# Kernel tuning notes

Hardware: AMD Instinct MI355X
Metric: run time of the kernel (lower is better)

The kernel has to match this reference:

```python
import jax, jax.numpy as jnp
import numpy as np

B, H, W, C = 8, 28, 28, 1024
NH = 16
HD = C // NH          # head dim 64
HID = 4 * C           # mlp hidden 4096
BC = C // 2           # bottleneck channels 512
SCALE = HD ** -0.5


def setup_inputs() -> dict:
    key = jax.random.key(0)
    ks = iter(jax.random.split(key, 32))
    def rn(shape, s=0.02):
        return jax.random.normal(next(ks), shape, jnp.float32) * s
    return dict(
        x=jax.random.normal(next(ks), (B, H, W, C), jnp.float32),
        norm1_w=jnp.ones((C,), jnp.float32), norm1_b=jnp.zeros((C,), jnp.float32),
        qkv_w=rn((C, 3 * C)), qkv_b=jnp.zeros((3 * C,), jnp.float32),
        proj_w=rn((C, C)), proj_b=jnp.zeros((C,), jnp.float32),
        rel_h=rn((2 * H - 1, HD)), rel_w=rn((2 * W - 1, HD)),
        norm2_w=jnp.ones((C,), jnp.float32), norm2_b=jnp.zeros((C,), jnp.float32),
        fc1_w=rn((C, HID)), fc1_b=jnp.zeros((HID,), jnp.float32),
        fc2_w=rn((HID, C)), fc2_b=jnp.zeros((C,), jnp.float32),
        conv1_w=rn((1, 1, C, BC)), ln1_w=jnp.ones((BC,), jnp.float32), ln1_b=jnp.zeros((BC,), jnp.float32),
        conv2_w=rn((3, 3, BC, BC)), ln2_w=jnp.ones((BC,), jnp.float32), ln2_b=jnp.zeros((BC,), jnp.float32),
        conv3_w=rn((1, 1, BC, C)), ln3_w=rn((C,)), ln3_b=rn((C,)),
    )


def _ln(x, w, b, eps):
    # layernorm over last axis (channels in NHWC)
    m = jnp.mean(x, -1, keepdims=True)
    v = jnp.mean((x - m) ** 2, -1, keepdims=True)
    return (x - m) * jax.lax.rsqrt(v + eps) * w + b


def _conv(x, w, pad):
    return jax.lax.conv_general_dilated(
        x, w, (1, 1), pad, dimension_numbers=('NHWC', 'HWIO', 'NHWC'))


def _gelu(x):
    return jax.nn.gelu(x, approximate=False)


def _block_forward(x, norm1_w, norm1_b, qkv_w, qkv_b, proj_w, proj_b,
                   rel_h, rel_w, norm2_w, norm2_b, fc1_w, fc1_b, fc2_w, fc2_b,
                   conv1_w, ln1_w, ln1_b, conv2_w, ln2_w, ln2_b, conv3_w, ln3_w, ln3_b):
    S = H * W
    shortcut = x
    xn = _ln(x, norm1_w, norm1_b, 1e-5)

    # ---- attention with decomposed relative position bias ----
    qkv = xn.reshape(B, S, C) @ qkv_w + qkv_b                 # [B,S,3C]
    qkv = qkv.reshape(B, S, 3, NH, HD).transpose(2, 0, 3, 1, 4)  # [3,B,nh,S,hd]
    q, k, v = qkv[0], qkv[1], qkv[2]
    attn = jnp.einsum('bnsd,bntd->bnst', q * SCALE, k)        # [B,nh,S,S]

    idx_h = jnp.arange(H)[:, None] - jnp.arange(H)[None, :] + (H - 1)
    idx_w = jnp.arange(W)[:, None] - jnp.arange(W)[None, :] + (W - 1)
    Rh = rel_h[idx_h]   # [H,H,hd]
    Rw = rel_w[idx_w]   # [W,W,hd]
    qr = q.reshape(B, NH, H, W, HD)
    bias_h = jnp.einsum('bnhwd,hkd->bnhwk', qr, Rh)           # [B,nh,H,W,H]
    bias_w = jnp.einsum('bnhwd,wkd->bnhwk', qr, Rw)           # [B,nh,H,W,W]
    attn = (attn.reshape(B, NH, H, W, H, W)
            + bias_h[..., :, None] + bias_w[..., None, :]).reshape(B, NH, S, S)

    attn = jax.nn.softmax(attn, axis=-1)
    out = jnp.einsum('bnst,bntd->bnsd', attn, v)              # [B,nh,S,hd]
    out = out.transpose(0, 2, 1, 3).reshape(B, H, W, C)
    out = out @ proj_w + proj_b

    x = shortcut + out

    # ---- MLP ----
    xn = _ln(x, norm2_w, norm2_b, 1e-5)
    x = x + (_gelu(xn.reshape(B, S, C) @ fc1_w + fc1_b) @ fc2_w + fc2_b).reshape(B, H, W, C)

    # ---- residual bottleneck conv (channel LayerNorm, eps=1e-6) ----
    out = _conv(x, conv1_w, 'VALID')
    out = _gelu(_ln(out, ln1_w, ln1_b, 1e-6))
    out = _conv(out, conv2_w, ((1, 1), (1, 1)))
    out = _gelu(_ln(out, ln2_w, ln2_b, 1e-6))
    out = _conv(out, conv3_w, 'VALID')
    out = _ln(out, ln3_w, ln3_b, 1e-6)
    return x + out


def reference(x, norm1_w, norm1_b, qkv_w, qkv_b, proj_w, proj_b,
              rel_h, rel_w, norm2_w, norm2_b, fc1_w, fc1_b, fc2_w, fc2_b,
              conv1_w, ln1_w, ln1_b, conv2_w, ln2_w, ln2_b, conv3_w, ln3_w, ln3_b):
    return _block_forward(x, norm1_w, norm1_b, qkv_w, qkv_b, proj_w, proj_b,
                          rel_h, rel_w, norm2_w, norm2_b, fc1_w, fc1_b, fc2_w, fc2_b,
                          conv1_w, ln1_w, ln1_b, conv2_w, ln2_w, ln2_b, conv3_w, ln3_w, ln3_b)
```

## Files before the change

### kernel.cpp

```cpp
#include <hip/hip_runtime.h>
#include <cstdint>
#include <cstddef>

using u16 = unsigned short;
using u32 = unsigned int;

__device__ __forceinline__ float bf2f(u16 u){
  union { u32 i; float f; } x; x.i = ((u32)u) << 16; return x.f;
}
__device__ __forceinline__ u16 f2bf(float f){
  union { float f; u32 i; } x; x.f = f;
  u32 r = x.i + 0x7fffu + ((x.i >> 16) & 1u);
  return (u16)(r >> 16);
}
__device__ __forceinline__ float gelu_f(float x){
  return 0.5f * x * (1.0f + erff(x * 0.70710678118654752f));
}
__device__ __forceinline__ void gld16(const void* g, void* l){
  __builtin_amdgcn_global_load_lds((__attribute__((address_space(1))) void*)(void*)g,
                                   (__attribute__((address_space(3))) void*)l, 16, 0, 0);
}

typedef __bf16 bf16x8 __attribute__((ext_vector_type(8)));
typedef float  f32x4  __attribute__((ext_vector_type(4)));
typedef u16    u16x4  __attribute__((ext_vector_type(4)));

__global__ __launch_bounds__(256) void k_transpose(const float* __restrict__ src,
                                                   u16* __restrict__ dst, int R, int C){
  __shared__ u16 tile[32][33];
  int bx = blockIdx.x * 32;
  int by = blockIdx.y * 32;
  int tx = threadIdx.x & 31;
  int ty = threadIdx.x >> 5;
  for (int r = ty; r < 32; r += 8)
    tile[r][tx] = f2bf(src[(size_t)(by + r) * C + bx + tx]);
  __syncthreads();
  for (int r = ty; r < 32; r += 8)
    dst[(size_t)(bx + r) * R + by + tx] = tile[tx][r];
}

template<bool IN_F32, bool DO_GELU>
__global__ __launch_bounds__(256) void k_layernorm(const void* __restrict__ inp,
    const float* __restrict__ w, const float* __restrict__ bsh,
    u16* __restrict__ out, int cols, float eps){
  int row = blockIdx.x, t = threadIdx.x;
  size_t base = (size_t)row * cols;
  const float* inf = (const float*)inp;
  const u16*  inb = (const u16*)inp;
  float v[4];
  int ep = cols >> 8;
  float s = 0.f, ss = 0.f;
  for (int e = 0; e < ep; ++e){
    int idx = t + (e << 8);
    float x = IN_F32 ? inf[base + idx] : bf2f(inb[base + idx]);
    v[e] = x; s += x; ss += x * x;
  }
#pragma unroll
  for (int off = 1; off < 64; off <<= 1){
    s  += __shfl_xor(s, off, 64);
    ss += __shfl_xor(ss, off, 64);
  }
  __shared__ float red[8];
  int wv = t >> 6;
  if ((t & 63) == 0){ red[wv] = s; red[4 + wv] = ss; }
  __syncthreads();
  s  = red[0] + red[1] + red[2] + red[3];
  ss = red[4] + red[5] + red[6] + red[7];
  float inv = 1.f / (float)cols;
  float mean = s * inv;
  float var = ss * inv - mean * mean;
  float rs = rsqrtf(var + eps);
  for (int e = 0; e < ep; ++e){
    int idx = t + (e << 8);
    float y = (v[e] - mean) * rs * w[idx] + bsh[idx];
    if (DO_GELU) y = gelu_f(y);
    out[base + idx] = f2bf(y);
  }
}

__global__ __launch_bounds__(256) void k_final(const u16* __restrict__ c3,
    const u16* __restrict__ x2, const float* __restrict__ w,
    const float* __restrict__ bsh, float* __restrict__ out){
  int row = blockIdx.x, t = threadIdx.x;
  size_t base = (size_t)row << 10;
  float v[4];
  float s = 0.f, ss = 0.f;
#pragma unroll
  for (int e = 0; e < 4; ++e){
    int idx = t + (e << 8);
    float x = bf2f(c3[base + idx]);
    v[e] = x; s += x; ss += x * x;
  }
#pragma unroll
  for (int off = 1; off < 64; off <<= 1){
    s  += __shfl_xor(s, off, 64);
    ss += __shfl_xor(ss, off, 64);
  }
  __shared__ float red[8];
  int wv = t >> 6;
  if ((t & 63) == 0){ red[wv] = s; red[4 + wv] = ss; }
  __syncthreads();
  s  = red[0] + red[1] + red[2] + red[3];
  ss = red[4] + red[5] + red[6] + red[7];
  float mean = s * (1.f/1024.f);
  float var = ss * (1.f/1024.f) - mean * mean;
  float rs = rsqrtf(var + 1e-6f);
#pragma unroll
  for (int e = 0; e < 4; ++e){
    int idx = t + (e << 8);
    float y = (v[e] - mean) * rs * w[idx] + bsh[idx];
    out[base + idx] = bf2f(x2[base + idx]) + y;
  }
}

template<bool BIAS, bool GELU, bool RES, bool OUTB, bool OUTF>
__global__ __launch_bounds__(256, 2) void k_gemm(
    const u16* __restrict__ A, const u16* __restrict__ Bt,
    const float* __restrict__ bias, const float* __restrict__ resf,
    u16* __restrict__ outb, float* __restrict__ outf, int N, int K)
{
  __shared__ __align__(16) u16 As[128 * 32];
  __shared__ __align__(16) u16 Bs[128 * 32];
  int t = threadIdx.x, lane = t & 63, wv = t >> 6;

  int nbx = gridDim.x;
  int nwg = nbx * gridDim.y;
  int li  = blockIdx.y * nbx + blockIdx.x;
  int qc = nwg >> 3, rc = nwg & 7;
  int xcd = li & 7, jj = li >> 3;
  int wg = (xcd < rc ? xcd * (qc + 1) : rc * (qc + 1) + (xcd - rc) * qc) + jj;
  int byy = wg / nbx;
  int bxx = wg - byy * nbx;
  int m0 = byy << 7, n0 = bxx << 7;

  int wm = (wv >> 1) << 6, wn = (wv & 1) << 6;

  f32x4 acc[4][4];
  const f32x4 z4 = {0.f, 0.f, 0.f, 0.f};
#pragma unroll
  for (int i = 0; i < 4; ++i)
#pragma unroll
    for (int j = 0; j < 4; ++j) acc[i][j] = z4;

  int srow = (wv << 5) + (lane >> 2);
  int skp  = (lane & 3) << 3;
  const u16* Ag = A  + (size_t)(m0 + srow) * K + skp;
  const u16* Bg = Bt + (size_t)(n0 + srow) * K + skp;
  u16* As0 = &As[(wv << 5) * 32];
  u16* As1 = As0 + 16 * 32;
  u16* Bs0 = &Bs[(wv << 5) * 32];
  u16* Bs1 = Bs0 + 16 * 32;
  const size_t rowskip = (size_t)16 * K;

  int fr = lane & 15, fq = (lane >> 4) << 3;

  for (int k0 = 0; k0 < K; k0 += 32){
    gld16(Ag + k0, As0);
    gld16(Ag + rowskip + k0, As1);
    gld16(Bg + k0, Bs0);
    gld16(Bg + rowskip + k0, Bs1);
    __syncthreads();
    bf16x8 af[4], bfr[4];
#pragma unroll
    for (int i = 0; i < 4; ++i)
      af[i] = *(const bf16x8*)&As[(wm + i * 16 + fr) * 32 + fq];
#pragma unroll
    for (int j = 0; j < 4; ++j)
      bfr[j] = *(const bf16x8*)&Bs[(wn + j * 16 + fr) * 32 + fq];
#pragma unroll
    for (int i = 0; i < 4; ++i)
#pragma unroll
      for (int j = 0; j < 4; ++j)
        acc[i][j] = __builtin_amdgcn_mfma_f32_16x16x32_bf16(af[i], bfr[j], acc[i][j], 0, 0, 0);
    __syncthreads();
  }

  int rr = (lane >> 4) << 2;
  int cc = lane & 15;
#pragma unroll
  for (int i = 0; i < 4; ++i)
#pragma unroll
    for (int j = 0; j < 4; ++j){
      int gc = n0 + wn + j * 16 + cc;
      float bb = BIAS ? bias[gc] : 0.f;
#pragma unroll
      for (int r = 0; r < 4; ++r){
        int gr = m0 + wm + i * 16 + rr + r;
        size_t idx = (size_t)gr * N + gc;
        float vv = acc[i][j][r] + bb;
        if (RES) vv += resf[idx];
        if (GELU) vv = gelu_f(vv);
        if (OUTF) outf[idx] = vv;
        if (OUTB) outb[idx] = f2bf(vv);
      }
    }
}

__global__ __launch_bounds__(256) void k_vtrans(const u16* __restrict__ qkv, u16* __restrict__ vtg){
  __shared__ u32 tile[64][33];
  int bnh = blockIdx.x;
  int st  = blockIdx.y;
  int b = bnh >> 4, nh = bnh & 15;
  int t = threadIdx.x;
  int tx = t & 31;
  int ty = t >> 5;
  const u16* src = qkv + (size_t)b * 784 * 3072 + 2048 + nh * 64;
  int s0 = st << 6;
  for (int r = ty; r < 64; r += 8){
    int s = s0 + r;
    u32 val = 0u;
    if (s < 784) val = *(const u32*)(src + (size_t)s * 3072 + tx * 2);
    tile[r][tx] = val;
  }
  __syncthreads();
  u16* dst = vtg + (size_t)bnh * 64 * 832 + s0;
  for (int d = ty; d < 64; d += 8){
    u32 lo = tile[2 * tx][d >> 1];
    u32 hi = tile[2 * tx + 1][d >> 1];
    u16 a  = (d & 1) ? (u16)(lo >> 16) : (u16)lo;
    u16 bb = (d & 1) ? (u16)(hi >> 16) : (u16)hi;
    u32 pk = (u32)a | ((u32)bb << 16);
    *(u32*)(dst + (size_t)d * 832 + 2 * tx) = pk;
  }
}

#define PST 72
#define GSTR 132
#define LOG2E 1.4426950408889634f
__global__ __launch_bounds__(256, 3) void k_attn7(const u16* __restrict__ qkv,
    const float* __restrict__ relh, const float* __restrict__ relw,
    const u16* __restrict__ vtg, u16* __restrict__ out)
{
  __shared__ __align__(16) u16 k_s[64 * 64];
  __shared__ __align__(16) u16 v_s[64 * 64];
  __shared__ __align__(16) u16 p_s[128 * PST];
  __shared__ __align__(16) u16 gh_t[28 * GSTR];
  __shared__ __align__(16) u16 gw_t[28 * GSTR];

  const int t = threadIdx.x, lane = t & 63, wv = t >> 6;
  int id = blockIdx.x;
  int xr = id & 7, rest = id >> 3;
  int qt = rest % 7, gg = rest / 7;
  int bnh = xr + (gg << 3);
  const int b = bnh >> 4, nh = bnh & 15;
  const int q0 = qt << 7;
  const size_t rowbase = (size_t)b * 784;
  const int wq0 = wv << 5;
  const int fr = lane & 15;
  const int fq = lane >> 4;

  u16* rh_s = p_s;
  u16* rw_s = p_s + 64 * PST;
  {
    int row = t >> 2, c0 = (t & 3) << 4;
    u16 bh_[16], bw_[16];
    if (row < 55){
      const float* ph = relh + row * 64 + c0;
      const float* pw = relw + row * 64 + c0;
#pragma unroll
      for (int e = 0; e < 16; ++e){ bh_[e] = f2bf(ph[e]); bw_[e] = f2bf(pw[e]); }
    } else {
#pragma unroll
      for (int e = 0; e < 16; ++e){ bh_[e] = 0; bw_[e] = 0; }
    }
    *(uint4*)&rh_s[row * PST + c0]     = *(uint4*)bh_;
    *(uint4*)&rh_s[row * PST + c0 + 8] = *(uint4*)(bh_ + 8);
    *(uint4*)&rw_s[row * PST + c0]     = *(uint4*)bw_;
    *(uint4*)&rw_s[row * PST + c0 + 8] = *(uint4*)(bw_ + 8);
  }

  bf16x8 qf[2][2];
#pragma unroll
  for (int mf = 0; mf < 2; ++mf)
#pragma unroll
    for (int ks = 0; ks < 2; ++ks){
      int row = q0 + wq0 + mf * 16 + fr;
      if (row < 784){
        qf[mf][ks] = *(const bf16x8*)(qkv + (rowbase + row) * 3072 + nh * 64 + fq * 8 + ks * 32);
      } else {
        uint4 z = {0u,0u,0u,0u}; qf[mf][ks] = *(bf16x8*)&z;
      }
    }
  __syncthreads();

  const f32x4 z4 = {0.f,0.f,0.f,0.f};
#pragma unroll
  for (int which = 0; which < 2; ++which){
    const u16* rs = which ? rw_s : rh_s;
    f32x4 G[2][4];
#pragma unroll
    for (int mf = 0; mf < 2; ++mf)
#pragma unroll
      for (int nf = 0; nf < 4; ++nf) G[mf][nf] = z4;
#pragma unroll
    for (int nf = 0; nf < 4; ++nf){
      bf16x8 rf0 = *(const bf16x8*)&rs[(nf * 16 + fr) * PST + fq * 8];
      bf16x8 rf1 = *(const bf16x8*)&rs[(nf * 16 + fr) * PST + fq * 8 + 32];
#pragma unroll
      for (int mf = 0; mf < 2; ++mf){
        G[mf][nf] = __builtin_amdgcn_mfma_f32_16x16x32_bf16(qf[mf][0], rf0, G[mf][nf], 0, 0, 0);
        G[mf][nf] = __builtin_amdgcn_mfma_f32_16x16x32_bf16(qf[mf][1], rf1, G[mf][nf], 0, 0, 0);
      }
    }
    u16* gt = which ? gw_t : gh_t;
#pragma unroll
    for (int mf = 0; mf < 2; ++mf)
#pragma unroll
      for (int r = 0; r < 4; ++r){
        int lr = wq0 + mf * 16 + fq * 4 + r;
        int grow = q0 + lr;
        int hq = grow / 28;
        int coord = which ? (grow - hq * 28) : hq;
#pragma unroll
        for (int nf = 0; nf < 4; ++nf){
          int j = nf * 16 + fr;
          int kk = coord + 27 - j;
          if ((unsigned)kk < 28u) gt[kk * GSTR + lr] = f2bf(G[mf][nf][r] * LOG2E);
        }
      }
  }
  __syncthreads();

  f32x4 acc[2][5];
#pragma unroll
  for (int mf = 0; mf < 2; ++mf)
#pragma unroll
    for (int nf = 0; nf < 5; ++nf) acc[mf][nf] = z4;

  u16 onesu[8];
#pragma unroll
  for (int e = 0; e < 8; ++e) onesu[e] = 0x3f80;
  bf16x8 onesf = *(bf16x8*)onesu;

  const int sr = lane >> 3;
  const int sc = (lane & 7) ^ sr;
  const u16* kstage = qkv + rowbase * 3072 + 1024 + nh * 64;
  const u16* vstage = vtg + (size_t)bnh * 64 * 832;
  const int r0 = (wv << 4) + sr;
  u16* kd0 = &k_s[(wv << 4) * 64];
  u16* kd1 = &k_s[((wv << 4) + 8) * 64];
  u16* vd0 = &v_s[(wv << 4) * 64];
  u16* vd1 = &v_s[((wv << 4) + 8) * 64];
  const int swz = (fr & 7);

  const float SSC = 0.125f * LOG2E;

  for (int kt = 0; kt < 13; ++kt){
    const int ktb = kt << 6;
    __syncthreads();
    {
      int jg0 = ktb + r0;       int jc0 = jg0 < 784 ? jg0 : 783;
      int jg1 = jg0 + 8;        int jc1 = jg1 < 784 ? jg1 : 783;
      gld16(kstage + (size_t)jc0 * 3072 + (sc << 3), kd0);
      gld16(kstage + (size_t)jc1 * 3072 + (sc << 3), kd1);
      gld16(vstage + (size_t)r0 * 832 + ktb + (sc << 3), vd0);
      gld16(vstage + (size_t)(r0 + 8) * 832 + ktb + (sc << 3), vd1);
    }
    __syncthreads();

    f32x4 S[2][4];
#pragma unroll
    for (int nf = 0; nf < 4; ++nf){
      int rb = (nf * 16 + fr) << 6;
      bf16x8 kf0 = *(const bf16x8*)&k_s[rb + ((fq ^ swz) << 3)];
      bf16x8 kf1 = *(const bf16x8*)&k_s[rb + (((fq + 4) ^ swz) << 3)];
#pragma unroll
      for (int mf = 0; mf < 2; ++mf){
        f32x4 s = z4;
        s = __builtin_amdgcn_mfma_f32_16x16x32_bf16(qf[mf][0], kf0, s, 0, 0, 0);
        s = __builtin_amdgcn_mfma_f32_16x16x32_bf16(qf[mf][1], kf1, s, 0, 0, 0);
        S[mf][nf] = s;
      }
    }

    int hj[4], wj[4]; bool val[4];
#pragma unroll
    for (int nf = 0; nf < 4; ++nf){
      int jg = ktb + nf * 16 + fr;
      int h = jg / 28;
      hj[nf] = h; wj[nf] = jg - h * 28; val[nf] = (jg < 784);
    }

#pragma unroll
    for (int mf = 0; mf < 2; ++mf){
      int lrb = wq0 + mf * 16 + fq * 4;
#pragma unroll
      for (int nf = 0; nf < 4; ++nf){
        u16x4 h4 = *(const u16x4*)&gh_t[hj[nf] * GSTR + lrb];
        u16x4 w4 = *(const u16x4*)&gw_t[wj[nf] * GSTR + lrb];
#pragma unroll
        for (int r = 0; r < 4; ++r){
          float p = 0.f;
          if (val[nf])
            p = exp2f(fmaf(SSC, S[mf][nf][r], bf2f(h4[r]) + bf2f(w4[r])));
          p_s[(lrb + r) * PST + nf * 16 + fr] = f2bf(p);
        }
      }
    }

#pragma unroll
    for (int ks = 0; ks < 2; ++ks){
      bf16x8 pf0 = *(const bf16x8*)&p_s[(wq0 + fr) * PST + fq * 8 + ks * 32];
      bf16x8 pf1 = *(const bf16x8*)&p_s[(wq0 + 16 + fr) * PST + fq * 8 + ks * 32];
#pragma unroll
      for (int nf = 0; nf < 4; ++nf){
        bf16x8 vf = *(const bf16x8*)&v_s[((nf * 16 + fr) << 6) + (((fq + ks * 4) ^ swz) << 3)];
        acc[0][nf] = __builtin_amdgcn_mfma_f32_16x16x32_bf16(pf0, vf, acc[0][nf], 0, 0, 0);
        acc[1][nf] = __builtin_amdgcn_mfma_f32_16x16x32_bf16(pf1, vf, acc[1][nf], 0, 0, 0);
      }
      acc[0][4] = __builtin_amdgcn_mfma_f32_16x16x32_bf16(pf0, onesf, acc[0][4], 0, 0, 0);
      acc[1][4] = __builtin_amdgcn_mfma_f32_16x16x32_bf16(pf1, onesf, acc[1][4], 0, 0, 0);
    }
  }

#pragma unroll
  for (int mf = 0; mf < 2; ++mf)
#pragma unroll
    for (int r = 0; r < 4; ++r){
      int row = q0 + wq0 + mf * 16 + fq * 4 + r;
      if (row < 784){
        float inv = 1.f / acc[mf][4][r];
        u16* dp = out + (rowbase + row) * 1024 + nh * 64 + fr;
#pragma unroll
        for (int nf = 0; nf < 4; ++nf)
          dp[nf * 16] = f2bf(acc[mf][nf][r] * inv);
      }
    }
}

__global__ __launch_bounds__(256) void k_im2col(const u16* __restrict__ g, u16* __restrict__ im){
  int idx = blockIdx.x * 256 + threadIdx.x;
  int p  = idx / 576;
  int c8 = idx - p * 576;
  int k0 = c8 << 3;
  int t9 = k0 >> 9;
  int ci = k0 & 511;
  int ky = t9 / 3, kx = t9 - ky * 3;
  int bb = p / 784;
  int s = p - bb * 784;
  int h = s / 28, w = s - h * 28;
  int hh = h + ky - 1, ww = w + kx - 1;
  uint4 val = make_uint4(0u, 0u, 0u, 0u);
  if ((unsigned)hh < 28u && (unsigned)ww < 28u)
    val = *(const uint4*)&g[(((size_t)(bb * 28 + hh)) * 28 + ww) * 512 + ci];
  *(uint4*)&im[(size_t)p * 4608 + k0] = val;
}

extern "C" void kernel_launch(void* const* d_in, const int* in_sizes, int n_in,
                              void* d_out, int out_size, void* d_ws, size_t ws_size,
                              hipStream_t stream)
{
  (void)in_sizes; (void)n_in; (void)out_size; (void)ws_size;
  const float* x      = (const float*)d_in[0];
  const float* n1w    = (const float*)d_in[1];
  const float* n1b    = (const float*)d_in[2];
  const float* qkv_w  = (const float*)d_in[3];
  const float* qkv_b  = (const float*)d_in[4];
  const float* proj_w = (const float*)d_in[5];
  const float* proj_b = (const float*)d_in[6];
  const float* rel_h  = (const float*)d_in[7];
  const float* rel_w  = (const float*)d_in[8];
  const float* n2w    = (const float*)d_in[9];
  const float* n2b    = (const float*)d_in[10];
  const float* fc1_w  = (const float*)d_in[11];
  const float* fc1_b  = (const float*)d_in[12];
  const float* fc2_w  = (const float*)d_in[13];
  const float* fc2_b  = (const float*)d_in[14];
  const float* c1w    = (const float*)d_in[15];
  const float* l1w    = (const float*)d_in[16];
  const float* l1b    = (const float*)d_in[17];
  const float* c2w    = (const float*)d_in[18];
  const float* l2w    = (const float*)d_in[19];
  const float* l2b    = (const float*)d_in[20];
  const float* c3w    = (const float*)d_in[21];
  const float* l3w    = (const float*)d_in[22];
  const float* l3b    = (const float*)d_in[23];

  char* ws = (char*)d_ws;
  size_t off = 0;
  auto alloc = [&](size_t bytes) -> void* {
    void* p = ws + off; off += (bytes + 255) & ~(size_t)255; return p;
  };
  const size_t M = 6272;
  u16* qkvT  = (u16*)alloc((size_t)3072 * 1024 * 2);
  u16* projT = (u16*)alloc((size_t)1024 * 1024 * 2);
  u16* fc1T  = (u16*)alloc((size_t)4096 * 1024 * 2);
  u16* fc2T  = (u16*)alloc((size_t)1024 * 4096 * 2);
  u16* c1T   = (u16*)alloc((size_t)512 * 1024 * 2);
  u16* c2T   = (u16*)alloc((size_t)512 * 4608 * 2);
  u16* c3T   = (u16*)alloc((size_t)1024 * 512 * 2);
  u16* qkvbuf = (u16*)alloc(M * 3072 * 2);
  u16* attn   = (u16*)alloc(M * 1024 * 2);
  u16* xn     = (u16*)alloc(M * 1024 * 2);
  float* x1   = (float*)alloc(M * 1024 * 4);
  u16* x2b    = (u16*)alloc(M * 1024 * 2);
  u16* c1buf  = (u16*)alloc(M * 512 * 2);
  u16* g1buf  = (u16*)alloc(M * 512 * 2);
  u16* hmlp   = qkvbuf;
  u16* im     = qkvbuf;
  u16* xn2    = xn;
  u16* c2buf  = c1buf;
  u16* g2buf  = g1buf;
  u16* c3buf  = attn;
  u16* vtg    = (u16*)x1;

  dim3 blk(256);
  k_transpose<<<dim3(3072/32, 1024/32), blk, 0, stream>>>(qkv_w, qkvT, 1024, 3072);
  k_transpose<<<dim3(1024/32, 1024/32), blk, 0, stream>>>(proj_w, projT, 1024, 1024);
  k_transpose<<<dim3(4096/32, 1024/32), blk, 0, stream>>>(fc1_w, fc1T, 1024, 4096);
  k_transpose<<<dim3(1024/32, 4096/32), blk, 0, stream>>>(fc2_w, fc2T, 4096, 1024);
  k_transpose<<<dim3(512/32, 1024/32),  blk, 0, stream>>>(c1w, c1T, 1024, 512);
  k_transpose<<<dim3(512/32, 4608/32),  blk, 0, stream>>>(c2w, c2T, 4608, 512);
  k_transpose<<<dim3(1024/32, 512/32),  blk, 0, stream>>>(c3w, c3T, 512, 1024);

  k_layernorm<true,false><<<6272, blk, 0, stream>>>(x, n1w, n1b, xn, 1024, 1e-5f);
  k_gemm<true,false,false,true,false><<<dim3(24,49), blk, 0, stream>>>(
      xn, qkvT, qkv_b, nullptr, qkvbuf, nullptr, 3072, 1024);
  k_vtrans<<<dim3(128, 13), blk, 0, stream>>>(qkvbuf, vtg);
  k_attn7<<<896, blk, 0, stream>>>(qkvbuf, rel_h, rel_w, vtg, attn);
  k_gemm<true,false,true,false,true><<<dim3(8,49), blk, 0, stream>>>(
      attn, projT, proj_b, x, nullptr, x1, 1024, 1024);
  k_layernorm<true,false><<<6272, blk, 0, stream>>>(x1, n2w, n2b, xn2, 1024, 1e-5f);
  k_gemm<true,true,false,true,false><<<dim3(32,49), blk, 0, stream>>>(
      xn2, fc1T, fc1_b, nullptr, hmlp, nullptr, 4096, 1024);
  k_gemm<true,false,true,true,false><<<dim3(8,49), blk, 0, stream>>>(
      hmlp, fc2T, fc2_b, x1, x2b, nullptr, 1024, 4096);
  k_gemm<false,false,false,true,false><<<dim3(4,49), blk, 0, stream>>>(
      x2b, c1T, nullptr, nullptr, c1buf, nullptr, 512, 1024);
  k_layernorm<false,true><<<6272, blk, 0, stream>>>(c1buf, l1w, l1b, g1buf, 512, 1e-6f);
  k_im2col<<<14112, blk, 0, stream>>>(g1buf, im);
  k_gemm<false,false,false,true,false><<<dim3(4,49), blk, 0, stream>>>(
      im, c2T, nullptr, nullptr, c2buf, nullptr, 512, 4608);
  k_layernorm<false,true><<<6272, blk, 0, stream>>>(c2buf, l2w, l2b, g2buf, 512, 1e-6f);
  k_gemm<false,false,false,true,false><<<dim3(8,49), blk, 0, stream>>>(
      g2buf, c3T, nullptr, nullptr, c3buf, nullptr, 1024, 512);
  k_final<<<6272, blk, 0, stream>>>(c3buf, x2b, l3w, l3b, (float*)d_out);
}
```

Before: 725.6 us.

## Double-buffer GEMM LDS loads, fuse im2col into conv GEMM, stage bf16 epilogue

The GEMM kernel now stages K-tiles into two LDS buffers, so the global-to-LDS loads for the next tile overlap the MFMA work on the current one. Waits use explicit vmcnt waitcnts and raw barriers. The 3x3 conv GEMM now builds its im2col addresses on the fly, reading padded taps from a zeroed scratch buffer, so the separate im2col kernel and its large intermediate buffer go away. Bf16 outputs are written through an LDS tile with 16-byte coalesced stores. The costs are double the LDS use, per-tile address arithmetic in the conv path, and an extra barrier in the epilogue.

```diff
diff --git a/kernel.cpp b/kernel.cpp
--- a/kernel.cpp
+++ b/kernel.cpp
@@ -113,14 +113,16 @@
   }
 }
 
-template<bool BIAS, bool GELU, bool RES, bool OUTB, bool OUTF>
+template<int DEPTH, bool BIAS, bool GELU, bool RES, bool OUTB, bool OUTF, bool CONV>
 __global__ __launch_bounds__(256, 2) void k_gemm(
     const u16* __restrict__ A, const u16* __restrict__ Bt,
     const float* __restrict__ bias, const float* __restrict__ resf,
-    u16* __restrict__ outb, float* __restrict__ outf, int N, int K)
+    u16* __restrict__ outb, float* __restrict__ outf,
+    const u16* __restrict__ zb, int N, int K)
 {
-  __shared__ __align__(16) u16 As[128 * 32];
-  __shared__ __align__(16) u16 Bs[128 * 32];
+  __shared__ __align__(16) u16 smem[DEPTH * 2 * 128 * 32];
+  u16* Asb = smem;
+  u16* Bsb = smem + DEPTH * 4096;
   int t = threadIdx.x, lane = t & 63, wv = t >> 6;
 
   int nbx = gridDim.x;
@@ -146,20 +148,44 @@
   int skp  = (lane & 3) << 3;
   const u16* Ag = A  + (size_t)(m0 + srow) * K + skp;
   const u16* Bg = Bt + (size_t)(n0 + srow) * K + skp;
-  u16* As0 = &As[(wv << 5) * 32];
-  u16* As1 = As0 + 16 * 32;
-  u16* Bs0 = &Bs[(wv << 5) * 32];
-  u16* Bs1 = Bs0 + 16 * 32;
   const size_t rowskip = (size_t)16 * K;
 
+  int bb0 = 0, h0 = 0, w0 = 0, bb1 = 0, h1 = 0, w1 = 0;
+  if (CONV){
+    int p0 = m0 + srow;
+    bb0 = p0 / 784; int s0i = p0 - bb0 * 784; h0 = s0i / 28; w0 = s0i - h0 * 28;
+    int p1 = p0 + 16;
+    bb1 = p1 / 784; int s1i = p1 - bb1 * 784; h1 = s1i / 28; w1 = s1i - h1 * 28;
+  }
+
   int fr = lane & 15, fq = (lane >> 4) << 3;
 
-  for (int k0 = 0; k0 < K; k0 += 32){
-    gld16(Ag + k0, As0);
-    gld16(Ag + rowskip + k0, As1);
-    gld16(Bg + k0, Bs0);
-    gld16(Bg + rowskip + k0, Bs1);
-    __syncthreads();
+  auto stage = [&](int buf, int k0){
+    u16* a0 = Asb + buf * 4096 + (wv << 5) * 32;
+    u16* b0 = Bsb + buf * 4096 + (wv << 5) * 32;
+    if (CONV){
+      int tap = k0 >> 9;
+      int ky = tap / 3, kx = tap - ky * 3;
+      int ci = (k0 & 511) + skp;
+      int hh0 = h0 + ky - 1, ww0 = w0 + kx - 1;
+      int hh1 = h1 + ky - 1, ww1 = w1 + kx - 1;
+      const u16* s0 = ((unsigned)hh0 < 28u && (unsigned)ww0 < 28u)
+          ? A + (((size_t)(bb0 * 28 + hh0)) * 28 + ww0) * 512 + ci : zb;
+      const u16* s1 = ((unsigned)hh1 < 28u && (unsigned)ww1 < 28u)
+          ? A + (((size_t)(bb1 * 28 + hh1)) * 28 + ww1) * 512 + ci : zb;
+      gld16(s0, a0);
+      gld16(s1, a0 + 16 * 32);
+    } else {
+      gld16(Ag + k0, a0);
+      gld16(Ag + rowskip + k0, a0 + 16 * 32);
+    }
+    gld16(Bg + k0, b0);
+    gld16(Bg + rowskip + k0, b0 + 16 * 32);
+  };
+
+  auto compute = [&](int buf){
+    const u16* As = Asb + buf * 4096;
+    const u16* Bs = Bsb + buf * 4096;
     bf16x8 af[4], bfr[4];
 #pragma unroll
     for (int i = 0; i < 4; ++i)
@@ -172,28 +198,70 @@
 #pragma unroll
       for (int j = 0; j < 4; ++j)
         acc[i][j] = __builtin_amdgcn_mfma_f32_16x16x32_bf16(af[i], bfr[j], acc[i][j], 0, 0, 0);
-    __syncthreads();
+  };
+
+  int nk = K >> 5;
+  stage(0, 0);
+
+  for (int kk = 0; kk < nk; ++kk){
+    int nxt = kk + 1;
+    if (nxt < nk){
+      stage(nxt & 1, nxt << 5);
+      asm volatile("s_waitcnt vmcnt(4)" ::: "memory");
+    } else {
+      asm volatile("s_waitcnt vmcnt(0)" ::: "memory");
+    }
+    __builtin_amdgcn_s_barrier();
+    compute(kk & 1);
+    __builtin_amdgcn_s_barrier();
   }
 
   int rr = (lane >> 4) << 2;
   int cc = lane & 15;
-#pragma unroll
-  for (int i = 0; i < 4; ++i)
-#pragma unroll
-    for (int j = 0; j < 4; ++j){
-      int gc = n0 + wn + j * 16 + cc;
-      float bb = BIAS ? bias[gc] : 0.f;
-#pragma unroll
-      for (int r = 0; r < 4; ++r){
-        int gr = m0 + wm + i * 16 + rr + r;
-        size_t idx = (size_t)gr * N + gc;
-        float vv = acc[i][j][r] + bb;
-        if (RES) vv += resf[idx];
-        if (GELU) vv = gelu_f(vv);
-        if (OUTF) outf[idx] = vv;
-        if (OUTB) outb[idx] = f2bf(vv);
-      }
-    }
+  if (OUTB){
+    u16* Cs = smem;
+#pragma unroll
+    for (int i = 0; i < 4; ++i)
+#pragma unroll
+      for (int j = 0; j < 4; ++j){
+        int lc = wn + j * 16 + cc;
+        int gc = n0 + lc;
+        float bb = BIAS ? bias[gc] : 0.f;
+#pragma unroll
+        for (int r = 0; r < 4; ++r){
+          int lr = wm + i * 16 + rr + r;
+          float vv = acc[i][j][r] + bb;
+          if (RES) vv += resf[(size_t)(m0 + lr) * N + gc];
+          if (GELU) vv = gelu_f(vv);
+          Cs[lr * 128 + lc] = f2bf(vv);
+        }
+      }
+    __syncthreads();
+#pragma unroll
+    for (int it = 0; it < 8; ++it){
+      int flat = it * 256 + t;
+      int row = flat >> 4;
+      int col = (flat & 15) << 3;
+      *(uint4*)&outb[(size_t)(m0 + row) * N + n0 + col] = *(const uint4*)&Cs[row * 128 + col];
+    }
+  } else {
+#pragma unroll
+    for (int i = 0; i < 4; ++i)
+#pragma unroll
+      for (int j = 0; j < 4; ++j){
+        int gc = n0 + wn + j * 16 + cc;
+        float bb = BIAS ? bias[gc] : 0.f;
+#pragma unroll
+        for (int r = 0; r < 4; ++r){
+          int gr = m0 + wm + i * 16 + rr + r;
+          size_t idx = (size_t)gr * N + gc;
+          float vv = acc[i][j][r] + bb;
+          if (RES) vv += resf[idx];
+          if (GELU) vv = gelu_f(vv);
+          outf[idx] = vv;
+        }
+      }
+  }
 }
 
 __global__ __launch_bounds__(256) void k_vtrans(const u16* __restrict__ qkv, u16* __restrict__ vtg){
@@ -426,24 +494,6 @@
           dp[nf * 16] = f2bf(acc[mf][nf][r] * inv);
       }
     }
-}
-
-__global__ __launch_bounds__(256) void k_im2col(const u16* __restrict__ g, u16* __restrict__ im){
-  int idx = blockIdx.x * 256 + threadIdx.x;
-  int p  = idx / 576;
-  int c8 = idx - p * 576;
-  int k0 = c8 << 3;
-  int t9 = k0 >> 9;
-  int ci = k0 & 511;
-  int ky = t9 / 3, kx = t9 - ky * 3;
-  int bb = p / 784;
-  int s = p - bb * 784;
-  int h = s / 28, w = s - h * 28;
-  int hh = h + ky - 1, ww = w + kx - 1;
-  uint4 val = make_uint4(0u, 0u, 0u, 0u);
-  if ((unsigned)hh < 28u && (unsigned)ww < 28u)
-    val = *(const uint4*)&g[(((size_t)(bb * 28 + hh)) * 28 + ww) * 512 + ci];
-  *(uint4*)&im[(size_t)p * 4608 + k0] = val;
 }
 
 extern "C" void kernel_launch(void* const* d_in, const int* in_sizes, int n_in,
@@ -496,13 +546,15 @@
   u16* x2b    = (u16*)alloc(M * 1024 * 2);
   u16* c1buf  = (u16*)alloc(M * 512 * 2);
   u16* g1buf  = (u16*)alloc(M * 512 * 2);
+  u16* zbuf   = (u16*)alloc(256);
   u16* hmlp   = qkvbuf;
-  u16* im     = qkvbuf;
   u16* xn2    = xn;
   u16* c2buf  = c1buf;
   u16* g2buf  = g1buf;
   u16* c3buf  = attn;
   u16* vtg    = (u16*)x1;
+
+  hipMemsetAsync(zbuf, 0, 256, stream);
 
   dim3 blk(256);
   k_transpose<<<dim3(3072/32, 1024/32), blk, 0, stream>>>(qkv_w, qkvT, 1024, 3072);
@@ -514,25 +566,24 @@
   k_transpose<<<dim3(1024/32, 512/32),  blk, 0, stream>>>(c3w, c3T, 512, 1024);
 
   k_layernorm<true,false><<<6272, blk, 0, stream>>>(x, n1w, n1b, xn, 1024, 1e-5f);
-  k_gemm<true,false,false,true,false><<<dim3(24,49), blk, 0, stream>>>(
-      xn, qkvT, qkv_b, nullptr, qkvbuf, nullptr, 3072, 1024);
+  k_gemm<2,true,false,false,true,false,false><<<dim3(24,49), blk, 0, stream>>>(
+      xn, qkvT, qkv_b, nullptr, qkvbuf, nullptr, nullptr, 3072, 1024);
   k_vtrans<<<dim3(128, 13), blk, 0, stream>>>(qkvbuf, vtg);
   k_attn7<<<896, blk, 0, stream>>>(qkvbuf, rel_h, rel_w, vtg, attn);
-  k_gemm<true,false,true,false,true><<<dim3(8,49), blk, 0, stream>>>(
-      attn, projT, proj_b, x, nullptr, x1, 1024, 1024);
+  k_gemm<2,true,false,true,false,true,false><<<dim3(8,49), blk, 0, stream>>>(
+      attn, projT, proj_b, x, nullptr, x1, nullptr, 1024, 1024);
   k_layernorm<true,false><<<6272, blk, 0, stream>>>(x1, n2w, n2b, xn2, 1024, 1e-5f);
-  k_gemm<true,true,false,true,false><<<dim3(32,49), blk, 0, stream>>>(
-      xn2, fc1T, fc1_b, nullptr, hmlp, nullptr, 4096, 1024);
-  k_gemm<true,false,true,true,false><<<dim3(8,49), blk, 0, stream>>>(
-      hmlp, fc2T, fc2_b, x1, x2b, nullptr, 1024, 4096);
-  k_gemm<false,false,false,true,false><<<dim3(4,49), blk, 0, stream>>>(
-      x2b, c1T, nullptr, nullptr, c1buf, nullptr, 512, 1024);
+  k_gemm<2,true,true,false,true,false,false><<<dim3(32,49), blk, 0, stream>>>(
+      xn2, fc1T, fc1_b, nullptr, hmlp, nullptr, nullptr, 4096, 1024);
+  k_gemm<2,true,false,true,true,false,false><<<dim3(8,49), blk, 0, stream>>>(
+      hmlp, fc2T, fc2_b, x1, x2b, nullptr, nullptr, 1024, 4096);
+  k_gemm<2,false,false,false,true,false,false><<<dim3(4,49), blk, 0, stream>>>(
+      x2b, c1T, nullptr, nullptr, c1buf, nullptr, nullptr, 512, 1024);
   k_layernorm<false,true><<<6272, blk, 0, stream>>>(c1buf, l1w, l1b, g1buf, 512, 1e-6f);
-  k_im2col<<<14112, blk, 0, stream>>>(g1buf, im);
-  k_gemm<false,false,false,true,false><<<dim3(4,49), blk, 0, stream>>>(
-      im, c2T, nullptr, nullptr, c2buf, nullptr, 512, 4608);
+  k_gemm<2,false,false,false,true,false,true><<<dim3(4,49), blk, 0, stream>>>(
+      g1buf, c2T, nullptr, nullptr, c2buf, nullptr, zbuf, 512, 4608);
   k_layernorm<false,true><<<6272, blk, 0, stream>>>(c2buf, l2w, l2b, g2buf, 512, 1e-6f);
-  k_gemm<false,false,false,true,false><<<dim3(8,49), blk, 0, stream>>>(
-      g2buf, c3T, nullptr, nullptr, c3buf, nullptr, 1024, 512);
+  k_gemm<2,false,false,false,true,false,false><<<dim3(8,49), blk, 0, stream>>>(
+      g2buf, c3T, nullptr, nullptr, c3buf, nullptr, nullptr, 1024, 512);
   k_final<<<6272, blk, 0, stream>>>(c3buf, x2b, l3w, l3b, (float*)d_out);
 }
```

Result: faster. 678.8 us (-6.4%).
